# Optimization experiments

Measured on AMD Instinct MI355X. Metric: run time of the kernel, lower is better.

The kernel has to match this reference:

```python
import jax, jax.numpy as jnp
import numpy as np

B, N, F, H, D, V = 1024, 64, 512, 512, 64, 16
NT = 6  # n_transform_params
SPLITS = [V * NT, NT, 1, V, V]
NOUT = sum(SPLITS)  # 135


def _make_transform(p):
    # p: [..., 6] -> similarity transform matrix [..., 3, 3], nonlinear=True
    sx, sy, theta, shear, tx, ty = [p[..., i] for i in range(6)]
    scale = jax.nn.sigmoid(sx) + 1e-2
    tx = jnp.tanh(tx * 5.0)
    ty = jnp.tanh(ty * 5.0)
    theta = theta * (2.0 * np.pi)
    c, s = jnp.cos(theta), jnp.sin(theta)
    zeros = jnp.zeros_like(scale)
    ones = jnp.ones_like(scale)
    row0 = jnp.stack([scale * c, -scale * s, tx], -1)
    row1 = jnp.stack([scale * s, scale * c, ty], -1)
    row2 = jnp.stack([zeros, zeros, ones], -1)
    return jnp.stack([row0, row1, row2], -2)


def setup_inputs() -> dict:
    key = jax.random.key(0)
    ks = jax.random.split(key, 12)
    feature = jax.random.normal(ks[0], (B, N, F), jnp.float32)
    # per-capsule feature MLP: F -> H -> D (with bias, ReLU between)
    mlp_w1 = jax.random.normal(ks[1], (N, F, H), jnp.float32) / np.sqrt(F)
    mlp_b1 = jnp.zeros((N, H), jnp.float32)
    mlp_w2 = jax.random.normal(ks[2], (N, H, D), jnp.float32) / np.sqrt(H)
    mlp_b2 = jnp.zeros((N, D), jnp.float32)
    # per-capsule caps MLP (bias=False): (D+1) -> H -> NOUT
    caps_w1 = jax.random.normal(ks[3], (N, D + 1, H), jnp.float32) / np.sqrt(D + 1)
    caps_w2 = jax.random.normal(ks[4], (N, H, NOUT), jnp.float32) / np.sqrt(H)
    # learned biases for outputs 1..4 and the static cpr
    bias_cvr = jnp.zeros((1, N, 1, NT), jnp.float32)
    bias_pl_caps = jnp.zeros((1, N, 1), jnp.float32)
    bias_pl_vote = jnp.zeros((1, N, V), jnp.float32)
    bias_scale = jnp.zeros((1, N, V), jnp.float32)
    cpr_static = jnp.zeros((1, N, V, NT), jnp.float32)
    return dict(feature=feature, mlp_w1=mlp_w1, mlp_b1=mlp_b1, mlp_w2=mlp_w2,
                mlp_b2=mlp_b2, caps_w1=caps_w1, caps_w2=caps_w2,
                bias_cvr=bias_cvr, bias_pl_caps=bias_pl_caps,
                bias_pl_vote=bias_pl_vote, bias_scale=bias_scale,
                cpr_static=cpr_static)


def reference(feature, mlp_w1, mlp_b1, mlp_w2, mlp_b2, caps_w1, caps_w2,
              bias_cvr, bias_pl_caps, bias_pl_vote, bias_scale, cpr_static):
    batch_size = feature.shape[0]
    # grouped per-capsule MLP over the capsule axis (replaces the python loop)
    h = jax.nn.relu(jnp.einsum('bnf,nfh->bnh', feature, mlp_w1) + mlp_b1[None])
    raw_caps_param = jnp.einsum('bnh,nhd->bnd', h, mlp_w2) + mlp_b2[None]  # [B,N,D]
    # dropout rate 0 -> caps_exist = ones
    caps_exist = jnp.ones((batch_size, N, 1), raw_caps_param.dtype)
    caps_param = jnp.concatenate([raw_caps_param, caps_exist], -1)  # [B,N,D+1]
    h2 = jax.nn.relu(jnp.einsum('bnd,ndh->bnh', caps_param, caps_w1))
    all_param = jnp.einsum('bnh,nho->bno', h2, caps_w2)  # [B,N,NOUT]
    offs = np.cumsum([0] + SPLITS)
    cpr_dynamic = all_param[..., offs[0]:offs[1]].reshape(batch_size, N, V, NT)
    cvr6 = all_param[..., offs[1]:offs[2]].reshape(batch_size, N, 1, NT)
    pl_caps = all_param[..., offs[2]:offs[3]].reshape(batch_size, N, 1)
    pl_vote = all_param[..., offs[3]:offs[4]].reshape(batch_size, N, V)
    scale6 = all_param[..., offs[4]:offs[5]].reshape(batch_size, N, V)
    cpr_dynamic_reg_loss = 0.5 * jnp.sum(cpr_dynamic ** 2) / batch_size
    cpr = _make_transform(cpr_dynamic + cpr_static)           # [B,N,V,3,3]
    cvr = _make_transform(cvr6 + bias_cvr)                     # [B,N,1,3,3]
    vote = jnp.matmul(cvr, cpr)                                # broadcast over V
    presence_logit_per_caps = pl_caps + bias_pl_caps
    presence_logit_per_vote = pl_vote + bias_pl_vote
    presence_per_vote = (jax.nn.sigmoid(presence_logit_per_caps)
                         * jax.nn.sigmoid(presence_logit_per_vote))
    # learn_vote_scale=True
    scale_per_vote = jax.nn.softplus(scale6 + bias_scale + 0.5) + 0.01
    return (vote, scale_per_vote, presence_per_vote,
            presence_logit_per_caps, presence_logit_per_vote,
            cpr_dynamic_reg_loss, raw_caps_param)
```

## Files before the change

### kernel.cpp

```cpp
#include <hip/hip_runtime.h>
#include <math.h>


#define BB    1024
#define NN    64
#define FF    512
#define HH    512
#define DD    64
#define VV    16
#define NTT   6
#define NOUTT 135

#define TBM     64
#define THREADS 512
#define NBLK    1024

typedef _Float16 f16;
typedef _Float16 f16x8 __attribute__((ext_vector_type(8)));
typedef float f32x4 __attribute__((ext_vector_type(4)));

#define MFMA16(a, b, c) __builtin_amdgcn_mfma_f32_16x16x32_f16((a), (b), (c), 0, 0, 0)

#define SZ_VOTE  ((size_t)BB*NN*VV*9)
#define OFF_VOTE  ((size_t)0)
#define OFF_SCALE (SZ_VOTE)
#define OFF_PRES  (OFF_SCALE + (size_t)BB*NN*VV)
#define OFF_PLC   (OFF_PRES  + (size_t)BB*NN*VV)
#define OFF_PLV   (OFF_PLC   + (size_t)BB*NN)
#define OFF_LOSS  (OFF_PLV   + (size_t)BB*NN*VV)
#define OFF_RAW   (OFF_LOSS  + 1)

#define WS_LOSSP 0
#define WS_W1H   ((size_t)8192)
#define WS_W2H   (WS_W1H  + 33554432)
#define WS_CW1H  (WS_W2H  + 4194304)
#define WS_CW2H  (WS_CW1H + 4194304)
#define WS_NEED  (WS_CW2H + 9437184)

__device__ __forceinline__ float sigmoidf_(float x) { return 1.f / (1.f + expf(-x)); }
__device__ __forceinline__ float softplusf_(float x) { return (x > 20.f) ? x : log1pf(expf(x)); }

__device__ __forceinline__ void make_tr(const float* p, float* M) {
  float scale = sigmoidf_(p[0]) + 1e-2f;
  float tx = tanhf(p[4] * 5.f);
  float ty = tanhf(p[5] * 5.f);
  float th = p[2] * 6.28318530717958647692f;
  float c = cosf(th), s = sinf(th);
  M[0] = scale * c; M[1] = -scale * s; M[2] = tx;
  M[3] = scale * s; M[4] =  scale * c; M[5] = ty;
  M[6] = 0.f;       M[7] = 0.f;        M[8] = 1.f;
}

__global__ void conv_fragB(const float* __restrict__ src, f16* __restrict__ dst,
                           int capStride, int Nsz, int Kc, int Nf) {
  const int tid = blockIdx.x * 256 + threadIdx.x;
  const int total = 64 * Kc * Nf * 64;
  if (tid >= total) return;
  const int c = tid & 15, g = (tid >> 4) & 3;
  int q = tid >> 6;
  const int nf = q % Nf; q /= Nf;
  const int kc = q % Kc; const int n = q / Kc;
  const int col = nf * 16 + c;
  const float* s = src + (size_t)n * capStride + (size_t)(kc * 32 + g * 8) * Nsz + col;
  f16x8 v;
  #pragma unroll
  for (int j = 0; j < 8; ++j) {
    float x = (col < Nsz) ? s[(size_t)j * Nsz] : 0.f;
    v[j] = (f16)x;
  }
  *(f16x8*)(dst + (size_t)tid * 8) = v;
}

__global__ __launch_bounds__(THREADS, 4)
void caps_mfma(const float* __restrict__ feature,
               const float* __restrict__ mlp_b1,
               const float* __restrict__ mlp_b2,
               const float* __restrict__ caps_w1,
               const f16*  __restrict__ w1h,
               const f16*  __restrict__ w2h,
               const f16*  __restrict__ cw1h,
               const f16*  __restrict__ cw2h,
               const float* __restrict__ bias_cvr,
               const float* __restrict__ bias_pl_caps,
               const float* __restrict__ bias_pl_vote,
               const float* __restrict__ bias_scale,
               const float* __restrict__ cpr_static,
               float* __restrict__ out,
               float* __restrict__ lossp)
{
  __shared__ __align__(16) f16 R0h[32768];
  __shared__ __align__(16) f16 Rraw[4096];
  __shared__ float red[8];

  const int t   = threadIdx.x;
  const int w   = t >> 6;
  const int ln  = t & 63;
  const int g   = ln >> 4;
  const int c16 = ln & 15;

  const int bid = blockIdx.x;
  const int xcd = bid & 7;
  const int j_  = bid >> 3;
  const int n   = (xcd << 3) + (j_ >> 4);
  const int b0  = (j_ & 15) * TBM;

  for (int rr = w; rr < 64; rr += 8) {
    const int mt = rr >> 4, kb = (rr & 15) * 4;
    const int koct = kb + g;
    const int brow = b0 + mt * 16 + c16;
    const float* fp = feature + ((size_t)brow * NN + n) * FF + koct * 8;
    const float4 f0 = *(const float4*)fp;
    const float4 f1 = *(const float4*)(fp + 4);
    f16x8 v;
    v[0]=(f16)f0.x; v[1]=(f16)f0.y; v[2]=(f16)f0.z; v[3]=(f16)f0.w;
    v[4]=(f16)f1.x; v[5]=(f16)f1.y; v[6]=(f16)f1.z; v[7]=(f16)f1.w;
    *(f16x8*)(R0h + mt * 8192 + koct * 128 + c16 * 8) = v;
  }
  __syncthreads();

  f32x4 acc[4][4];
  #pragma unroll
  for (int mt = 0; mt < 4; ++mt)
    #pragma unroll
    for (int nf = 0; nf < 4; ++nf) acc[mt][nf] = (f32x4)0.f;

  {
    const f16* wp = w1h + (size_t)n * 16 * 16384 + (size_t)(w * 4) * 512 + (size_t)ln * 8;
    f16x8 bA[4], bB[4];
    #pragma unroll
    for (int nf = 0; nf < 4; ++nf) bA[nf] = *(const f16x8*)(wp + (size_t)nf * 512);
    #pragma unroll
    for (int kc = 0; kc < 16; kc += 2) {
      #pragma unroll
      for (int nf = 0; nf < 4; ++nf)
        bB[nf] = *(const f16x8*)(wp + (size_t)(kc + 1) * 16384 + (size_t)nf * 512);
      f16x8 af[4];
      #pragma unroll
      for (int mt = 0; mt < 4; ++mt)
        af[mt] = *(const f16x8*)(R0h + mt * 8192 + (kc * 4 + g) * 128 + c16 * 8);
      #pragma unroll
      for (int nf = 0; nf < 4; ++nf)
        #pragma unroll
        for (int mt = 0; mt < 4; ++mt)
          acc[mt][nf] = MFMA16(af[mt], bA[nf], acc[mt][nf]);
      if (kc + 2 < 16) {
        #pragma unroll
        for (int nf = 0; nf < 4; ++nf)
          bA[nf] = *(const f16x8*)(wp + (size_t)(kc + 2) * 16384 + (size_t)nf * 512);
      }
      #pragma unroll
      for (int mt = 0; mt < 4; ++mt)
        af[mt] = *(const f16x8*)(R0h + mt * 8192 + ((kc + 1) * 4 + g) * 128 + c16 * 8);
      #pragma unroll
      for (int nf = 0; nf < 4; ++nf)
        #pragma unroll
        for (int mt = 0; mt < 4; ++mt)
          acc[mt][nf] = MFMA16(af[mt], bB[nf], acc[mt][nf]);
    }
  }
  __syncthreads();

  {
    const float* b1n = mlp_b1 + (size_t)n * HH;
    #pragma unroll
    for (int nf = 0; nf < 4; ++nf) {
      const int hcol = w * 64 + nf * 16 + c16;
      const float bb = b1n[hcol];
      const int koct = hcol >> 3, jj = hcol & 7;
      #pragma unroll
      for (int mt = 0; mt < 4; ++mt)
        #pragma unroll
        for (int r = 0; r < 4; ++r)
          R0h[mt * 8192 + koct * 128 + (g * 4 + r) * 8 + jj] =
              (f16)fmaxf(acc[mt][nf][r] + bb, 0.f);
    }
  }
  __syncthreads();

  {
    const int dnf = w & 3, mh = w >> 2;
    f32x4 accB0 = (f32x4)0.f, accB1 = (f32x4)0.f;
    const f16* w2p = w2h + (size_t)n * 16 * 2048 + (size_t)dnf * 512 + (size_t)ln * 8;
    f16x8 bw[16];
    #pragma unroll
    for (int kc = 0; kc < 16; ++kc) bw[kc] = *(const f16x8*)(w2p + (size_t)kc * 2048);
    #pragma unroll
    for (int kc = 0; kc < 16; ++kc) {
      const f16x8 af0 = *(const f16x8*)(R0h + (2 * mh)     * 8192 + (kc * 4 + g) * 128 + c16 * 8);
      const f16x8 af1 = *(const f16x8*)(R0h + (2 * mh + 1) * 8192 + (kc * 4 + g) * 128 + c16 * 8);
      accB0 = MFMA16(af0, bw[kc], accB0);
      accB1 = MFMA16(af1, bw[kc], accB1);
    }
    const int d = dnf * 16 + c16;
    const float bb2 = mlp_b2[(size_t)n * DD + d];
    const int koct = d >> 3, jj = d & 7;
    #pragma unroll
    for (int i = 0; i < 2; ++i) {
      const int mt = 2 * mh + i;
      const f32x4 a = i ? accB1 : accB0;
      #pragma unroll
      for (int r = 0; r < 4; ++r) {
        const int m = mt * 16 + g * 4 + r;
        const float v = a[r] + bb2;
        out[OFF_RAW + (((size_t)(b0 + m)) * NN + n) * DD + d] = v;
        Rraw[mt * 1024 + koct * 128 + (g * 4 + r) * 8 + jj] = (f16)v;
      }
    }
  }
  __syncthreads();

  #pragma unroll
  for (int mt = 0; mt < 4; ++mt)
    #pragma unroll
    for (int nf = 0; nf < 4; ++nf) acc[mt][nf] = (f32x4)0.f;
  {
    const f16* cw1p = cw1h + (size_t)n * 2 * 16384 + (size_t)(w * 4) * 512 + (size_t)ln * 8;
    f16x8 bc0[4], bc1[4];
    #pragma unroll
    for (int nf = 0; nf < 4; ++nf) bc0[nf] = *(const f16x8*)(cw1p + (size_t)nf * 512);
    #pragma unroll
    for (int nf = 0; nf < 4; ++nf) bc1[nf] = *(const f16x8*)(cw1p + 16384 + (size_t)nf * 512);
    #pragma unroll
    for (int kc = 0; kc < 2; ++kc) {
      f16x8 af[4];
      #pragma unroll
      for (int mt = 0; mt < 4; ++mt)
        af[mt] = *(const f16x8*)(Rraw + mt * 1024 + (kc * 4 + g) * 128 + c16 * 8);
      #pragma unroll
      for (int nf = 0; nf < 4; ++nf)
        #pragma unroll
        for (int mt = 0; mt < 4; ++mt)
          acc[mt][nf] = MFMA16(af[mt], kc ? bc1[nf] : bc0[nf], acc[mt][nf]);
    }
    const float* cl = caps_w1 + ((size_t)n * 65 + 64) * HH;
    #pragma unroll
    for (int nf = 0; nf < 4; ++nf) {
      const int hcol = w * 64 + nf * 16 + c16;
      const float ev = cl[hcol];
      const int koct = hcol >> 3, jj = hcol & 7;
      #pragma unroll
      for (int mt = 0; mt < 4; ++mt)
        #pragma unroll
        for (int r = 0; r < 4; ++r)
          R0h[mt * 8192 + koct * 128 + (g * 4 + r) * 8 + jj] =
              (f16)fmaxf(acc[mt][nf][r] + ev, 0.f);
    }
  }
  __syncthreads();

  f32x4 accD[4];
  f32x4 accD8[4];
  #pragma unroll
  for (int mt = 0; mt < 4; ++mt) { accD[mt] = (f32x4)0.f; accD8[mt] = (f32x4)0.f; }
  {
    const f16* cw2p = cw2h + (size_t)n * 16 * 4608 + (size_t)ln * 8;
    const bool w0 = (w == 0);
    f16x8 dA, dB, dA8, dB8;
    dA = *(const f16x8*)(cw2p + (size_t)w * 512);
    if (w0) dA8 = *(const f16x8*)(cw2p + (size_t)8 * 512);
    #pragma unroll
    for (int kc = 0; kc < 16; kc += 2) {
      dB = *(const f16x8*)(cw2p + (size_t)(kc + 1) * 4608 + (size_t)w * 512);
      if (w0) dB8 = *(const f16x8*)(cw2p + (size_t)(kc + 1) * 4608 + (size_t)8 * 512);
      f16x8 af[4];
      #pragma unroll
      for (int mt = 0; mt < 4; ++mt)
        af[mt] = *(const f16x8*)(R0h + mt * 8192 + (kc * 4 + g) * 128 + c16 * 8);
      #pragma unroll
      for (int mt = 0; mt < 4; ++mt) accD[mt] = MFMA16(af[mt], dA, accD[mt]);
      if (w0) {
        #pragma unroll
        for (int mt = 0; mt < 4; ++mt) accD8[mt] = MFMA16(af[mt], dA8, accD8[mt]);
      }
      if (kc + 2 < 16) {
        dA = *(const f16x8*)(cw2p + (size_t)(kc + 2) * 4608 + (size_t)w * 512);
        if (w0) dA8 = *(const f16x8*)(cw2p + (size_t)(kc + 2) * 4608 + (size_t)8 * 512);
      }
      #pragma unroll
      for (int mt = 0; mt < 4; ++mt)
        af[mt] = *(const f16x8*)(R0h + mt * 8192 + ((kc + 1) * 4 + g) * 128 + c16 * 8);
      #pragma unroll
      for (int mt = 0; mt < 4; ++mt) accD[mt] = MFMA16(af[mt], dB, accD[mt]);
      if (w0) {
        #pragma unroll
        for (int mt = 0; mt < 4; ++mt) accD8[mt] = MFMA16(af[mt], dB8, accD8[mt]);
      }
    }
  }
  __syncthreads();

  float* apf = (float*)R0h;
  {
    const int col = w * 16 + c16;
    #pragma unroll
    for (int mt = 0; mt < 4; ++mt)
      #pragma unroll
      for (int r = 0; r < 4; ++r)
        apf[(size_t)(mt * 16 + g * 4 + r) * 145 + col] = accD[mt][r];
    if (w == 0) {
      const int col8 = 128 + c16;
      if (col8 < NOUTT) {
        #pragma unroll
        for (int mt = 0; mt < 4; ++mt)
          #pragma unroll
          for (int r = 0; r < 4; ++r)
            apf[(size_t)(mt * 16 + g * 4 + r) * 145 + col8] = accD8[mt][r];
      }
    }
  }
  __syncthreads();

  {
    const int mrow = t >> 3, seg = t & 7;
    const float* ar = apf + (size_t)mrow * 145 + seg * 12;
    float ls = 0.f;
    #pragma unroll
    for (int i = 0; i < 12; ++i) ls += ar[i] * ar[i];
    ls += __shfl_down(ls, 32); ls += __shfl_down(ls, 16); ls += __shfl_down(ls, 8);
    ls += __shfl_down(ls, 4);  ls += __shfl_down(ls, 2);  ls += __shfl_down(ls, 1);
    if (ln == 0) red[w] = ls;
    __syncthreads();
    if (t == 0) {
      float s = 0.f;
      #pragma unroll
      for (int i = 0; i < 8; ++i) s += red[i];
      lossp[bid] = s;
    }
  }

  for (int vt = t; vt < TBM * VV; vt += THREADS) {
    const int m = vt >> 4;
    const int v = vt & 15;
    const float* aprow = apf + (size_t)m * 145;
    float pd[6], pc[6];
    #pragma unroll
    for (int ii = 0; ii < 6; ++ii)
      pd[ii] = aprow[v * NTT + ii] + cpr_static[((size_t)n * VV + v) * NTT + ii];
    #pragma unroll
    for (int ii = 0; ii < 6; ++ii)
      pc[ii] = aprow[96 + ii] + bias_cvr[(size_t)n * NTT + ii];
    float Ma[9], Mb[9], Mv[9];
    make_tr(pc, Ma);
    make_tr(pd, Mb);
    #pragma unroll
    for (int r = 0; r < 3; ++r)
      #pragma unroll
      for (int c = 0; c < 3; ++c)
        Mv[r * 3 + c] = Ma[r*3+0] * Mb[0*3+c] + Ma[r*3+1] * Mb[1*3+c] + Ma[r*3+2] * Mb[2*3+c];
    const int b = b0 + m;
    const size_t vbase = (((size_t)b * NN + n) * VV + v) * 9;
    #pragma unroll
    for (int k = 0; k < 9; ++k) out[OFF_VOTE + vbase + k] = Mv[k];
    const size_t sidx = ((size_t)b * NN + n) * VV + v;
    out[OFF_SCALE + sidx] = softplusf_(aprow[119 + v] + bias_scale[(size_t)n * VV + v] + 0.5f) + 0.01f;
    const float plv = aprow[103 + v] + bias_pl_vote[(size_t)n * VV + v];
    out[OFF_PLV + sidx] = plv;
    const float plc = aprow[102] + bias_pl_caps[n];
    if (v == 0) out[OFF_PLC + (size_t)b * NN + n] = plc;
    out[OFF_PRES + sidx] = sigmoidf_(plc) * sigmoidf_(plv);
  }
}

struct SA  { float featT[16][36]; float w1c[16][512]; };
struct SBp { float hbuf[32][128]; float w2c[128][64]; };
struct SC  { float cpT[64][32];  float cw1c[16][512]; };
struct SD  { float h2buf[32][68]; float cw2c[64][168]; };
struct SP  { float ap[32][136]; };
union  SH  { SA a; SBp b; SC c; SD d; SP p; };

__global__ __launch_bounds__(256)
void caps_fp32(const float* __restrict__ feature, const float* __restrict__ mlp_w1,
               const float* __restrict__ mlp_b1, const float* __restrict__ mlp_w2,
               const float* __restrict__ mlp_b2, const float* __restrict__ caps_w1,
               const float* __restrict__ caps_w2, const float* __restrict__ bias_cvr,
               const float* __restrict__ bias_pl_caps, const float* __restrict__ bias_pl_vote,
               const float* __restrict__ bias_scale, const float* __restrict__ cpr_static,
               float* __restrict__ out, float* __restrict__ lossp)
{
  __shared__ SH sh;
  __shared__ float red4[4];
  const int t  = threadIdx.x;
  const int wv = t >> 6;
  const int ln = t & 63;
  const int m0 = wv << 3;
  const int cA0 = ln << 2;
  const int cA1 = 256 + (ln << 2);
  const int bid   = blockIdx.x;
  const int xcd   = bid & 7;
  const int j     = bid >> 3;
  const int n     = (xcd << 3) + (j >> 5);
  const int mtile = j & 31;
  const int b0    = mtile * 32;

  float acc[64];
  #pragma unroll
  for (int i = 0; i < 64; ++i) acc[i] = 0.f;
  {
    const float* w1n = mlp_w1 + (size_t)n * FF * HH;
    for (int k0 = 0; k0 < FF; k0 += 16) {
      for (int e = t; e < 512; e += 256) {
        const int mm = e >> 4, kk = e & 15;
        sh.a.featT[kk][mm] = feature[(((size_t)(b0 + mm)) * NN + n) * FF + (k0 + kk)];
      }
      { const float4* src = (const float4*)(w1n + (size_t)k0 * HH);
        float4* dst = (float4*)sh.a.w1c;
        for (int u = t; u < 2048; u += 256) dst[u] = src[u]; }
      __syncthreads();
      #pragma unroll 4
      for (int kk = 0; kk < 16; ++kk) {
        const float4 a0  = *(const float4*)&sh.a.featT[kk][m0];
        const float4 a1  = *(const float4*)&sh.a.featT[kk][m0 + 4];
        const float4 bv0 = *(const float4*)&sh.a.w1c[kk][cA0];
        const float4 bv1 = *(const float4*)&sh.a.w1c[kk][cA1];
        const float av[8] = {a0.x, a0.y, a0.z, a0.w, a1.x, a1.y, a1.z, a1.w};
        const float bv[8] = {bv0.x, bv0.y, bv0.z, bv0.w, bv1.x, bv1.y, bv1.z, bv1.w};
        #pragma unroll
        for (int i = 0; i < 8; ++i)
          #pragma unroll
          for (int c = 0; c < 8; ++c) acc[i * 8 + c] += av[i] * bv[c];
      }
      __syncthreads();
    }
    const float* b1n = mlp_b1 + (size_t)n * HH;
    const float4 bb0 = *(const float4*)&b1n[cA0];
    const float4 bb1 = *(const float4*)&b1n[cA1];
    const float bb[8] = {bb0.x, bb0.y, bb0.z, bb0.w, bb1.x, bb1.y, bb1.z, bb1.w};
    #pragma unroll
    for (int i = 0; i < 8; ++i)
      #pragma unroll
      for (int c = 0; c < 8; ++c) acc[i * 8 + c] = fmaxf(acc[i * 8 + c] + bb[c], 0.f);
  }
  float rac[8];
  #pragma unroll
  for (int i = 0; i < 8; ++i) rac[i] = 0.f;
  {
    const float4* w2base = (const float4*)(mlp_w2 + (size_t)n * HH * DD);
    for (int q = 0; q < 4; ++q) {
      if (q == (ln >> 5)) {
        const int lc = (ln & 31) << 2;
        #pragma unroll
        for (int i = 0; i < 8; ++i)
          *(float4*)&sh.b.hbuf[m0 + i][lc] = make_float4(acc[i*8+0], acc[i*8+1], acc[i*8+2], acc[i*8+3]);
      }
      if (q == 2 + (ln >> 5)) {
        const int lc = (ln & 31) << 2;
        #pragma unroll
        for (int i = 0; i < 8; ++i)
          *(float4*)&sh.b.hbuf[m0 + i][lc] = make_float4(acc[i*8+4], acc[i*8+5], acc[i*8+6], acc[i*8+7]);
      }
      { const float4* src = w2base + (size_t)q * 2048;
        float4* dst = (float4*)sh.b.w2c;
        for (int u = t; u < 2048; u += 256) dst[u] = src[u]; }
      __syncthreads();
      #pragma unroll 2
      for (int kk = 0; kk < 128; kk += 4) {
        const float w0  = sh.b.w2c[kk + 0][ln];
        const float w1_ = sh.b.w2c[kk + 1][ln];
        const float w2_ = sh.b.w2c[kk + 2][ln];
        const float w3_ = sh.b.w2c[kk + 3][ln];
        #pragma unroll
        for (int i = 0; i < 8; ++i) {
          const float4 h4 = *(const float4*)&sh.b.hbuf[m0 + i][kk];
          rac[i] += h4.x * w0 + h4.y * w1_ + h4.z * w2_ + h4.w * w3_;
        }
      }
      __syncthreads();
    }
    const float bb2 = mlp_b2[(size_t)n * DD + ln];
    #pragma unroll
    for (int i = 0; i < 8; ++i) {
      const float rv = rac[i] + bb2;
      out[OFF_RAW + (((size_t)(b0 + m0 + i)) * NN + n) * DD + ln] = rv;
      sh.c.cpT[ln][(m0 + i + ln) & 31] = rv;
    }
  }
  #pragma unroll
  for (int i = 0; i < 64; ++i) acc[i] = 0.f;
  {
    const float* cw1n = caps_w1 + (size_t)n * (DD + 1) * HH;
    for (int k0 = 0; k0 < 64; k0 += 16) {
      const float4* src = (const float4*)(cw1n + (size_t)k0 * HH);
      float4* dst = (float4*)sh.c.cw1c;
      for (int u = t; u < 2048; u += 256) dst[u] = src[u];
      __syncthreads();
      #pragma unroll 4
      for (int kk = 0; kk < 16; ++kk) {
        const int k = k0 + kk;
        float av[8];
        #pragma unroll
        for (int i = 0; i < 8; ++i) av[i] = sh.c.cpT[k][(m0 + i + k) & 31];
        const float4 bv0 = *(const float4*)&sh.c.cw1c[kk][cA0];
        const float4 bv1 = *(const float4*)&sh.c.cw1c[kk][cA1];
        const float bv[8] = {bv0.x, bv0.y, bv0.z, bv0.w, bv1.x, bv1.y, bv1.z, bv1.w};
        #pragma unroll
        for (int i = 0; i < 8; ++i)
          #pragma unroll
          for (int c = 0; c < 8; ++c) acc[i * 8 + c] += av[i] * bv[c];
      }
      __syncthreads();
    }
    const float* cl = cw1n + (size_t)64 * HH;
    const float4 e0 = *(const float4*)&cl[cA0];
    const float4 e1 = *(const float4*)&cl[cA1];
    const float ev[8] = {e0.x, e0.y, e0.z, e0.w, e1.x, e1.y, e1.z, e1.w};
    #pragma unroll
    for (int i = 0; i < 8; ++i)
      #pragma unroll
      for (int c = 0; c < 8; ++c) acc[i * 8 + c] = fmaxf(acc[i * 8 + c] + ev[c], 0.f);
  }
  float ap[17];
  #pragma unroll
  for (int i = 0; i < 17; ++i) ap[i] = 0.f;
  const int mD = t >> 3;
  const int cD = t & 7;
  {
    const float* cw2n = caps_w2 + (size_t)n * HH * NOUTT;
    for (int q = 0; q < 8; ++q) {
      if (q == (ln >> 4)) {
        const int lc = (ln & 15) << 2;
        #pragma unroll
        for (int i = 0; i < 8; ++i)
          *(float4*)&sh.d.h2buf[m0 + i][lc] = make_float4(acc[i*8+0], acc[i*8+1], acc[i*8+2], acc[i*8+3]);
      }
      if (q == 4 + (ln >> 4)) {
        const int lc = (ln & 15) << 2;
        #pragma unroll
        for (int i = 0; i < 8; ++i)
          *(float4*)&sh.d.h2buf[m0 + i][lc] = make_float4(acc[i*8+4], acc[i*8+5], acc[i*8+6], acc[i*8+7]);
      }
      { const float* wsrc = cw2n + (size_t)(q << 6) * NOUTT;
        for (int r = wv; r < 64; r += 4)
          for (int c = ln; c < NOUTT; c += 64)
            sh.d.cw2c[r][c + ((c >> 4) << 2)] = wsrc[(size_t)r * NOUTT + c]; }
      __syncthreads();
      const int base20 = 20 * cD;
      #pragma unroll 2
      for (int kk = 0; kk < 64; ++kk) {
        const float hv = sh.d.h2buf[mD][kk];
        const float4 wa = *(const float4*)&sh.d.cw2c[kk][base20 + 0];
        const float4 wb = *(const float4*)&sh.d.cw2c[kk][base20 + 4];
        const float4 wc = *(const float4*)&sh.d.cw2c[kk][base20 + 8];
        const float4 wd = *(const float4*)&sh.d.cw2c[kk][base20 + 12];
        ap[0]  += hv * wa.x; ap[1]  += hv * wa.y; ap[2]  += hv * wa.z; ap[3]  += hv * wa.w;
        ap[4]  += hv * wb.x; ap[5]  += hv * wb.y; ap[6]  += hv * wb.z; ap[7]  += hv * wb.w;
        ap[8]  += hv * wc.x; ap[9]  += hv * wc.y; ap[10] += hv * wc.z; ap[11] += hv * wc.w;
        ap[12] += hv * wd.x; ap[13] += hv * wd.y; ap[14] += hv * wd.z; ap[15] += hv * wd.w;
        if (cD < 7) ap[16] += hv * sh.d.cw2c[kk][160 + cD];
      }
      __syncthreads();
    }
  }
  #pragma unroll
  for (int i = 0; i < 16; ++i) sh.p.ap[mD][(cD << 4) + i] = ap[i];
  if (cD < 7) sh.p.ap[mD][128 + cD] = ap[16];
  float ls = 0.f;
  if (cD < 6) {
    #pragma unroll
    for (int i = 0; i < 16; ++i) ls += ap[i] * ap[i];
  }
  __syncthreads();
  ls += __shfl_down(ls, 32); ls += __shfl_down(ls, 16); ls += __shfl_down(ls, 8);
  ls += __shfl_down(ls, 4);  ls += __shfl_down(ls, 2);  ls += __shfl_down(ls, 1);
  if (ln == 0) red4[wv] = ls;
  __syncthreads();
  if (t == 0) lossp[bid] = red4[0] + red4[1] + red4[2] + red4[3];
  for (int vt = t; vt < 32 * VV; vt += 256) {
    const int m = vt >> 4;
    const int v = vt & 15;
    const float* aprow = sh.p.ap[m];
    float pd[6], pc[6];
    #pragma unroll
    for (int ii = 0; ii < 6; ++ii)
      pd[ii] = aprow[v * NTT + ii] + cpr_static[((size_t)n * VV + v) * NTT + ii];
    #pragma unroll
    for (int ii = 0; ii < 6; ++ii)
      pc[ii] = aprow[96 + ii] + bias_cvr[(size_t)n * NTT + ii];
    float Ma[9], Mb[9], Mv[9];
    make_tr(pc, Ma);
    make_tr(pd, Mb);
    #pragma unroll
    for (int r = 0; r < 3; ++r)
      #pragma unroll
      for (int c = 0; c < 3; ++c)
        Mv[r * 3 + c] = Ma[r*3+0] * Mb[0*3+c] + Ma[r*3+1] * Mb[1*3+c] + Ma[r*3+2] * Mb[2*3+c];
    const int b = b0 + m;
    const size_t vbase = (((size_t)b * NN + n) * VV + v) * 9;
    #pragma unroll
    for (int k = 0; k < 9; ++k) out[OFF_VOTE + vbase + k] = Mv[k];
    const size_t sidx = ((size_t)b * NN + n) * VV + v;
    out[OFF_SCALE + sidx] = softplusf_(aprow[119 + v] + bias_scale[(size_t)n * VV + v] + 0.5f) + 0.01f;
    const float plv = aprow[103 + v] + bias_pl_vote[(size_t)n * VV + v];
    out[OFF_PLV + sidx] = plv;
    const float plc = aprow[102] + bias_pl_caps[n];
    if (v == 0) out[OFF_PLC + (size_t)b * NN + n] = plc;
    out[OFF_PRES + sidx] = sigmoidf_(plc) * sigmoidf_(plv);
  }
}

__global__ __launch_bounds__(256)
void loss_reduce(const float* __restrict__ lossp, float* __restrict__ out, int nblk) {
  __shared__ float r2[4];
  const int t = threadIdx.x;
  float s = 0.f;
  for (int i = t; i < nblk; i += 256) s += lossp[i];
  s += __shfl_down(s, 32); s += __shfl_down(s, 16); s += __shfl_down(s, 8);
  s += __shfl_down(s, 4);  s += __shfl_down(s, 2);  s += __shfl_down(s, 1);
  if ((t & 63) == 0) r2[t >> 6] = s;
  __syncthreads();
  if (t == 0) out[OFF_LOSS] = (r2[0] + r2[1] + r2[2] + r2[3]) * (0.5f / 1024.f);
}

extern "C" void kernel_launch(void* const* d_in, const int* in_sizes, int n_in,
                              void* d_out, int out_size, void* d_ws, size_t ws_size,
                              hipStream_t stream) {
  (void)in_sizes; (void)n_in; (void)out_size;
  const float* feature      = (const float*)d_in[0];
  const float* mlp_w1       = (const float*)d_in[1];
  const float* mlp_b1       = (const float*)d_in[2];
  const float* mlp_w2       = (const float*)d_in[3];
  const float* mlp_b2       = (const float*)d_in[4];
  const float* caps_w1      = (const float*)d_in[5];
  const float* caps_w2      = (const float*)d_in[6];
  const float* bias_cvr     = (const float*)d_in[7];
  const float* bias_pl_caps = (const float*)d_in[8];
  const float* bias_pl_vote = (const float*)d_in[9];
  const float* bias_scale   = (const float*)d_in[10];
  const float* cpr_static   = (const float*)d_in[11];
  float* out   = (float*)d_out;
  float* lossp = (float*)d_ws;

  if (ws_size >= WS_NEED) {
    f16* w1h  = (f16*)((char*)d_ws + WS_W1H);
    f16* w2h  = (f16*)((char*)d_ws + WS_W2H);
    f16* cw1h = (f16*)((char*)d_ws + WS_CW1H);
    f16* cw2h = (f16*)((char*)d_ws + WS_CW2H);
    hipLaunchKernelGGL(conv_fragB, dim3(2097152 / 256), dim3(256), 0, stream,
                       mlp_w1, w1h, 512 * 512, 512, 16, 32);
    hipLaunchKernelGGL(conv_fragB, dim3(262144 / 256), dim3(256), 0, stream,
                       mlp_w2, w2h, 512 * 64, 64, 16, 4);
    hipLaunchKernelGGL(conv_fragB, dim3(262144 / 256), dim3(256), 0, stream,
                       caps_w1, cw1h, 65 * 512, 512, 2, 32);
    hipLaunchKernelGGL(conv_fragB, dim3(589824 / 256), dim3(256), 0, stream,
                       caps_w2, cw2h, 512 * 135, 135, 16, 9);
    hipLaunchKernelGGL(caps_mfma, dim3(NBLK), dim3(THREADS), 0, stream,
                       feature, mlp_b1, mlp_b2, caps_w1, w1h, w2h, cw1h, cw2h,
                       bias_cvr, bias_pl_caps, bias_pl_vote, bias_scale, cpr_static,
                       out, lossp);
    hipLaunchKernelGGL(loss_reduce, dim3(1), dim3(256), 0, stream, lossp, out, NBLK);
  } else {
    hipLaunchKernelGGL(caps_fp32, dim3(2048), dim3(256), 0, stream,
                       feature, mlp_w1, mlp_b1, mlp_w2, mlp_b2, caps_w1, caps_w2,
                       bias_cvr, bias_pl_caps, bias_pl_vote, bias_scale, cpr_static,
                       out, lossp);
    hipLaunchKernelGGL(loss_reduce, dim3(1), dim3(256), 0, stream, lossp, out, 2048);
  }
}
```

Baseline: 168.3 us.

## Split hidden dimension into two halves to shrink LDS and raise occupancy

Restructures the fused capsule MLP kernel so the 512-wide hidden layer is computed in two 256-column passes. The first layer streams the input features in two K halves through a smaller shared buffer, and the second-layer products accumulate across passes. This cuts shared memory use from 64KB to about 37KB and halves the per-wave accumulator registers, allowing launch bounds of 6 blocks per CU instead of 4. In exchange it adds more barriers, reloads the feature tile per pass, and uses a triple-buffered weight prefetch.

```diff
diff --git a/kernel.cpp b/kernel.cpp
--- a/kernel.cpp
+++ b/kernel.cpp
@@ -71,7 +71,7 @@
   *(f16x8*)(dst + (size_t)tid * 8) = v;
 }
 
-__global__ __launch_bounds__(THREADS, 4)
+__global__ __launch_bounds__(THREADS, 6)
 void caps_mfma(const float* __restrict__ feature,
                const float* __restrict__ mlp_b1,
                const float* __restrict__ mlp_b2,
@@ -88,9 +88,10 @@
                float* __restrict__ out,
                float* __restrict__ lossp)
 {
-  __shared__ __align__(16) f16 R0h[32768];
+  __shared__ __align__(16) float RbigF[9280];
   __shared__ __align__(16) f16 Rraw[4096];
   __shared__ float red[8];
+  f16* RB = (f16*)RbigF;
 
   const int t   = threadIdx.x;
   const int w   = t >> 6;
@@ -104,192 +105,199 @@
   const int n   = (xcd << 3) + (j_ >> 4);
   const int b0  = (j_ & 15) * TBM;
 
-  for (int rr = w; rr < 64; rr += 8) {
-    const int mt = rr >> 4, kb = (rr & 15) * 4;
-    const int koct = kb + g;
-    const int brow = b0 + mt * 16 + c16;
-    const float* fp = feature + ((size_t)brow * NN + n) * FF + koct * 8;
-    const float4 f0 = *(const float4*)fp;
-    const float4 f1 = *(const float4*)(fp + 4);
-    f16x8 v;
-    v[0]=(f16)f0.x; v[1]=(f16)f0.y; v[2]=(f16)f0.z; v[3]=(f16)f0.w;
-    v[4]=(f16)f1.x; v[5]=(f16)f1.y; v[6]=(f16)f1.z; v[7]=(f16)f1.w;
-    *(f16x8*)(R0h + mt * 8192 + koct * 128 + c16 * 8) = v;
-  }
-  __syncthreads();
-
-  f32x4 acc[4][4];
-  #pragma unroll
-  for (int mt = 0; mt < 4; ++mt)
-    #pragma unroll
-    for (int nf = 0; nf < 4; ++nf) acc[mt][nf] = (f32x4)0.f;
+  const int dnf = w & 3, mh = w >> 2;
+
+  f32x4 accB[2];
+  accB[0] = (f32x4)0.f; accB[1] = (f32x4)0.f;
+
+  for (int cp = 0; cp < 2; ++cp) {
+    f32x4 acc[4][2];
+    #pragma unroll
+    for (int mt = 0; mt < 4; ++mt) { acc[mt][0] = (f32x4)0.f; acc[mt][1] = (f32x4)0.f; }
+
+    for (int kh = 0; kh < 2; ++kh) {
+      #pragma unroll
+      for (int rr4 = 0; rr4 < 4; ++rr4) {
+        const int rr = rr4 * 8 + w;
+        const int mt = rr >> 3, kb = (rr & 7) * 4;
+        const int koctl = kb + g;
+        const int brow = b0 + mt * 16 + c16;
+        const float* fp = feature + ((size_t)brow * NN + n) * FF + (size_t)(kh * 32 + koctl) * 8;
+        const float4 f0 = *(const float4*)fp;
+        const float4 f1 = *(const float4*)(fp + 4);
+        f16x8 v;
+        v[0]=(f16)f0.x; v[1]=(f16)f0.y; v[2]=(f16)f0.z; v[3]=(f16)f0.w;
+        v[4]=(f16)f1.x; v[5]=(f16)f1.y; v[6]=(f16)f1.z; v[7]=(f16)f1.w;
+        *(f16x8*)(RB + mt * 4096 + koctl * 128 + c16 * 8) = v;
+      }
+      __syncthreads();
+
+      const f16* wp = w1h + (size_t)n * 262144 + (size_t)(cp * 16 + 2 * w) * 512 + (size_t)ln * 8;
+      f16x8 bb[3][2];
+      #pragma unroll
+      for (int d = 0; d < 2; ++d) {
+        bb[0][d] = *(const f16x8*)(wp + (size_t)(kh * 8 + 0) * 16384 + (size_t)d * 512);
+        bb[1][d] = *(const f16x8*)(wp + (size_t)(kh * 8 + 1) * 16384 + (size_t)d * 512);
+      }
+      #pragma unroll
+      for (int kcl = 0; kcl < 8; ++kcl) {
+        const int slot = kcl % 3;
+        f16x8 af[4];
+        #pragma unroll
+        for (int mt = 0; mt < 4; ++mt)
+          af[mt] = *(const f16x8*)(RB + mt * 4096 + (kcl * 4 + g) * 128 + c16 * 8);
+        #pragma unroll
+        for (int d = 0; d < 2; ++d)
+          #pragma unroll
+          for (int mt = 0; mt < 4; ++mt)
+            acc[mt][d] = MFMA16(af[mt], bb[slot][d], acc[mt][d]);
+        if (kcl + 2 < 8) {
+          const int s2 = (kcl + 2) % 3;
+          #pragma unroll
+          for (int d = 0; d < 2; ++d)
+            bb[s2][d] = *(const f16x8*)(wp + (size_t)(kh * 8 + kcl + 2) * 16384 + (size_t)d * 512);
+        }
+      }
+      __syncthreads();
+    }
+
+    f16x8 bw[8];
+    {
+      const f16* w2p = w2h + (size_t)n * 32768 + (size_t)dnf * 512 + (size_t)ln * 8;
+      #pragma unroll
+      for (int kcl = 0; kcl < 8; ++kcl)
+        bw[kcl] = *(const f16x8*)(w2p + (size_t)(cp * 8 + kcl) * 2048);
+    }
+
+    {
+      const float* b1n = mlp_b1 + (size_t)n * HH;
+      #pragma unroll
+      for (int d = 0; d < 2; ++d) {
+        const int hcol = cp * 256 + w * 32 + d * 16 + c16;
+        const float bbv = b1n[hcol];
+        const int lc = w * 32 + d * 16 + c16;
+        const int koctl = lc >> 3, jj = lc & 7;
+        #pragma unroll
+        for (int mt = 0; mt < 4; ++mt)
+          #pragma unroll
+          for (int r = 0; r < 4; ++r)
+            RB[mt * 4096 + koctl * 128 + (g * 4 + r) * 8 + jj] =
+                (f16)fmaxf(acc[mt][d][r] + bbv, 0.f);
+      }
+    }
+    __syncthreads();
+
+    #pragma unroll
+    for (int kcl = 0; kcl < 8; ++kcl) {
+      const f16x8 a0 = *(const f16x8*)(RB + (2 * mh)     * 4096 + (kcl * 4 + g) * 128 + c16 * 8);
+      const f16x8 a1 = *(const f16x8*)(RB + (2 * mh + 1) * 4096 + (kcl * 4 + g) * 128 + c16 * 8);
+      accB[0] = MFMA16(a0, bw[kcl], accB[0]);
+      accB[1] = MFMA16(a1, bw[kcl], accB[1]);
+    }
+    __syncthreads();
+  }
 
   {
-    const f16* wp = w1h + (size_t)n * 16 * 16384 + (size_t)(w * 4) * 512 + (size_t)ln * 8;
-    f16x8 bA[4], bB[4];
-    #pragma unroll
-    for (int nf = 0; nf < 4; ++nf) bA[nf] = *(const f16x8*)(wp + (size_t)nf * 512);
-    #pragma unroll
-    for (int kc = 0; kc < 16; kc += 2) {
-      #pragma unroll
-      for (int nf = 0; nf < 4; ++nf)
-        bB[nf] = *(const f16x8*)(wp + (size_t)(kc + 1) * 16384 + (size_t)nf * 512);
-      f16x8 af[4];
-      #pragma unroll
-      for (int mt = 0; mt < 4; ++mt)
-        af[mt] = *(const f16x8*)(R0h + mt * 8192 + (kc * 4 + g) * 128 + c16 * 8);
-      #pragma unroll
-      for (int nf = 0; nf < 4; ++nf)
-        #pragma unroll
-        for (int mt = 0; mt < 4; ++mt)
-          acc[mt][nf] = MFMA16(af[mt], bA[nf], acc[mt][nf]);
-      if (kc + 2 < 16) {
-        #pragma unroll
-        for (int nf = 0; nf < 4; ++nf)
-          bA[nf] = *(const f16x8*)(wp + (size_t)(kc + 2) * 16384 + (size_t)nf * 512);
-      }
-      #pragma unroll
-      for (int mt = 0; mt < 4; ++mt)
-        af[mt] = *(const f16x8*)(R0h + mt * 8192 + ((kc + 1) * 4 + g) * 128 + c16 * 8);
-      #pragma unroll
-      for (int nf = 0; nf < 4; ++nf)
-        #pragma unroll
-        for (int mt = 0; mt < 4; ++mt)
-          acc[mt][nf] = MFMA16(af[mt], bB[nf], acc[mt][nf]);
-    }
-  }
-  __syncthreads();
-
-  {
-    const float* b1n = mlp_b1 + (size_t)n * HH;
-    #pragma unroll
-    for (int nf = 0; nf < 4; ++nf) {
-      const int hcol = w * 64 + nf * 16 + c16;
-      const float bb = b1n[hcol];
-      const int koct = hcol >> 3, jj = hcol & 7;
-      #pragma unroll
-      for (int mt = 0; mt < 4; ++mt)
-        #pragma unroll
-        for (int r = 0; r < 4; ++r)
-          R0h[mt * 8192 + koct * 128 + (g * 4 + r) * 8 + jj] =
-              (f16)fmaxf(acc[mt][nf][r] + bb, 0.f);
-    }
-  }
-  __syncthreads();
-
-  {
-    const int dnf = w & 3, mh = w >> 2;
-    f32x4 accB0 = (f32x4)0.f, accB1 = (f32x4)0.f;
-    const f16* w2p = w2h + (size_t)n * 16 * 2048 + (size_t)dnf * 512 + (size_t)ln * 8;
-    f16x8 bw[16];
-    #pragma unroll
-    for (int kc = 0; kc < 16; ++kc) bw[kc] = *(const f16x8*)(w2p + (size_t)kc * 2048);
-    #pragma unroll
-    for (int kc = 0; kc < 16; ++kc) {
-      const f16x8 af0 = *(const f16x8*)(R0h + (2 * mh)     * 8192 + (kc * 4 + g) * 128 + c16 * 8);
-      const f16x8 af1 = *(const f16x8*)(R0h + (2 * mh + 1) * 8192 + (kc * 4 + g) * 128 + c16 * 8);
-      accB0 = MFMA16(af0, bw[kc], accB0);
-      accB1 = MFMA16(af1, bw[kc], accB1);
-    }
-    const int d = dnf * 16 + c16;
-    const float bb2 = mlp_b2[(size_t)n * DD + d];
-    const int koct = d >> 3, jj = d & 7;
+    const int dcol = dnf * 16 + c16;
+    const float bb2 = mlp_b2[(size_t)n * DD + dcol];
+    const int koct = dcol >> 3, jj = dcol & 7;
     #pragma unroll
     for (int i = 0; i < 2; ++i) {
       const int mt = 2 * mh + i;
-      const f32x4 a = i ? accB1 : accB0;
+      const f32x4 a = i ? accB[1] : accB[0];
       #pragma unroll
       for (int r = 0; r < 4; ++r) {
         const int m = mt * 16 + g * 4 + r;
         const float v = a[r] + bb2;
-        out[OFF_RAW + (((size_t)(b0 + m)) * NN + n) * DD + d] = v;
+        out[OFF_RAW + (((size_t)(b0 + m)) * NN + n) * DD + dcol] = v;
         Rraw[mt * 1024 + koct * 128 + (g * 4 + r) * 8 + jj] = (f16)v;
       }
     }
   }
   __syncthreads();
 
-  #pragma unroll
-  for (int mt = 0; mt < 4; ++mt)
-    #pragma unroll
-    for (int nf = 0; nf < 4; ++nf) acc[mt][nf] = (f32x4)0.f;
-  {
-    const f16* cw1p = cw1h + (size_t)n * 2 * 16384 + (size_t)(w * 4) * 512 + (size_t)ln * 8;
-    f16x8 bc0[4], bc1[4];
-    #pragma unroll
-    for (int nf = 0; nf < 4; ++nf) bc0[nf] = *(const f16x8*)(cw1p + (size_t)nf * 512);
-    #pragma unroll
-    for (int nf = 0; nf < 4; ++nf) bc1[nf] = *(const f16x8*)(cw1p + 16384 + (size_t)nf * 512);
-    #pragma unroll
-    for (int kc = 0; kc < 2; ++kc) {
-      f16x8 af[4];
-      #pragma unroll
-      for (int mt = 0; mt < 4; ++mt)
-        af[mt] = *(const f16x8*)(Rraw + mt * 1024 + (kc * 4 + g) * 128 + c16 * 8);
-      #pragma unroll
-      for (int nf = 0; nf < 4; ++nf)
-        #pragma unroll
-        for (int mt = 0; mt < 4; ++mt)
-          acc[mt][nf] = MFMA16(af[mt], kc ? bc1[nf] : bc0[nf], acc[mt][nf]);
-    }
-    const float* cl = caps_w1 + ((size_t)n * 65 + 64) * HH;
-    #pragma unroll
-    for (int nf = 0; nf < 4; ++nf) {
-      const int hcol = w * 64 + nf * 16 + c16;
-      const float ev = cl[hcol];
-      const int koct = hcol >> 3, jj = hcol & 7;
-      #pragma unroll
-      for (int mt = 0; mt < 4; ++mt)
-        #pragma unroll
-        for (int r = 0; r < 4; ++r)
-          R0h[mt * 8192 + koct * 128 + (g * 4 + r) * 8 + jj] =
-              (f16)fmaxf(acc[mt][nf][r] + ev, 0.f);
-    }
-  }
-  __syncthreads();
-
-  f32x4 accD[4];
-  f32x4 accD8[4];
+  f32x4 accD[4], accD8[4];
   #pragma unroll
   for (int mt = 0; mt < 4; ++mt) { accD[mt] = (f32x4)0.f; accD8[mt] = (f32x4)0.f; }
-  {
-    const f16* cw2p = cw2h + (size_t)n * 16 * 4608 + (size_t)ln * 8;
-    const bool w0 = (w == 0);
-    f16x8 dA, dB, dA8, dB8;
-    dA = *(const f16x8*)(cw2p + (size_t)w * 512);
-    if (w0) dA8 = *(const f16x8*)(cw2p + (size_t)8 * 512);
-    #pragma unroll
-    for (int kc = 0; kc < 16; kc += 2) {
-      dB = *(const f16x8*)(cw2p + (size_t)(kc + 1) * 4608 + (size_t)w * 512);
-      if (w0) dB8 = *(const f16x8*)(cw2p + (size_t)(kc + 1) * 4608 + (size_t)8 * 512);
-      f16x8 af[4];
-      #pragma unroll
-      for (int mt = 0; mt < 4; ++mt)
-        af[mt] = *(const f16x8*)(R0h + mt * 8192 + (kc * 4 + g) * 128 + c16 * 8);
-      #pragma unroll
-      for (int mt = 0; mt < 4; ++mt) accD[mt] = MFMA16(af[mt], dA, accD[mt]);
+  const bool w0 = (w == 0);
+
+  for (int cp = 0; cp < 2; ++cp) {
+    f32x4 accC[4][2];
+    #pragma unroll
+    for (int mt = 0; mt < 4; ++mt) { accC[mt][0] = (f32x4)0.f; accC[mt][1] = (f32x4)0.f; }
+    {
+      const f16* cw1p = cw1h + (size_t)n * 32768 + (size_t)(cp * 16 + 2 * w) * 512 + (size_t)ln * 8;
+      f16x8 bc[2][2];
+      #pragma unroll
+      for (int kc = 0; kc < 2; ++kc)
+        #pragma unroll
+        for (int d = 0; d < 2; ++d)
+          bc[kc][d] = *(const f16x8*)(cw1p + (size_t)kc * 16384 + (size_t)d * 512);
+      #pragma unroll
+      for (int kc = 0; kc < 2; ++kc) {
+        f16x8 af[4];
+        #pragma unroll
+        for (int mt = 0; mt < 4; ++mt)
+          af[mt] = *(const f16x8*)(Rraw + mt * 1024 + (kc * 4 + g) * 128 + c16 * 8);
+        #pragma unroll
+        for (int d = 0; d < 2; ++d)
+          #pragma unroll
+          for (int mt = 0; mt < 4; ++mt)
+            accC[mt][d] = MFMA16(af[mt], bc[kc][d], accC[mt][d]);
+      }
+    }
+    {
+      const float* cl = caps_w1 + ((size_t)n * 65 + 64) * HH;
+      #pragma unroll
+      for (int d = 0; d < 2; ++d) {
+        const int hcol = cp * 256 + w * 32 + d * 16 + c16;
+        const float ev = cl[hcol];
+        const int lc = w * 32 + d * 16 + c16;
+        const int koctl = lc >> 3, jj = lc & 7;
+        #pragma unroll
+        for (int mt = 0; mt < 4; ++mt)
+          #pragma unroll
+          for (int r = 0; r < 4; ++r)
+            RB[mt * 4096 + koctl * 128 + (g * 4 + r) * 8 + jj] =
+                (f16)fmaxf(accC[mt][d][r] + ev, 0.f);
+      }
+    }
+    __syncthreads();
+
+    {
+      const f16* cw2p = cw2h + (size_t)n * 73728 + (size_t)ln * 8;
+      f16x8 db[3], db8[3];
+      db[0] = *(const f16x8*)(cw2p + (size_t)(cp * 8 + 0) * 4608 + (size_t)w * 512);
+      db[1] = *(const f16x8*)(cw2p + (size_t)(cp * 8 + 1) * 4608 + (size_t)w * 512);
       if (w0) {
-        #pragma unroll
-        for (int mt = 0; mt < 4; ++mt) accD8[mt] = MFMA16(af[mt], dA8, accD8[mt]);
-      }
-      if (kc + 2 < 16) {
-        dA = *(const f16x8*)(cw2p + (size_t)(kc + 2) * 4608 + (size_t)w * 512);
-        if (w0) dA8 = *(const f16x8*)(cw2p + (size_t)(kc + 2) * 4608 + (size_t)8 * 512);
-      }
-      #pragma unroll
-      for (int mt = 0; mt < 4; ++mt)
-        af[mt] = *(const f16x8*)(R0h + mt * 8192 + ((kc + 1) * 4 + g) * 128 + c16 * 8);
-      #pragma unroll
-      for (int mt = 0; mt < 4; ++mt) accD[mt] = MFMA16(af[mt], dB, accD[mt]);
-      if (w0) {
-        #pragma unroll
-        for (int mt = 0; mt < 4; ++mt) accD8[mt] = MFMA16(af[mt], dB8, accD8[mt]);
-      }
-    }
-  }
-  __syncthreads();
-
-  float* apf = (float*)R0h;
+        db8[0] = *(const f16x8*)(cw2p + (size_t)(cp * 8 + 0) * 4608 + (size_t)8 * 512);
+        db8[1] = *(const f16x8*)(cw2p + (size_t)(cp * 8 + 1) * 4608 + (size_t)8 * 512);
+      }
+      #pragma unroll
+      for (int kcl = 0; kcl < 8; ++kcl) {
+        const int slot = kcl % 3;
+        f16x8 af[4];
+        #pragma unroll
+        for (int mt = 0; mt < 4; ++mt)
+          af[mt] = *(const f16x8*)(RB + mt * 4096 + (kcl * 4 + g) * 128 + c16 * 8);
+        #pragma unroll
+        for (int mt = 0; mt < 4; ++mt) accD[mt] = MFMA16(af[mt], db[slot], accD[mt]);
+        if (w0) {
+          #pragma unroll
+          for (int mt = 0; mt < 4; ++mt) accD8[mt] = MFMA16(af[mt], db8[slot], accD8[mt]);
+        }
+        if (kcl + 2 < 8) {
+          const int s2 = (kcl + 2) % 3;
+          db[s2] = *(const f16x8*)(cw2p + (size_t)(cp * 8 + kcl + 2) * 4608 + (size_t)w * 512);
+          if (w0)
+            db8[s2] = *(const f16x8*)(cw2p + (size_t)(cp * 8 + kcl + 2) * 4608 + (size_t)8 * 512);
+        }
+      }
+    }
+    __syncthreads();
+  }
+
+  float* apf = RbigF;
   {
     const int col = w * 16 + c16;
     #pragma unroll
@@ -297,7 +305,7 @@
       #pragma unroll
       for (int r = 0; r < 4; ++r)
         apf[(size_t)(mt * 16 + g * 4 + r) * 145 + col] = accD[mt][r];
-    if (w == 0) {
+    if (w0) {
       const int col8 = 128 + c16;
       if (col8 < NOUTT) {
         #pragma unroll
```

Result: slower. 276.1 us (+64.1%).
